# Kernel optimization log

Measured on AMD Instinct MI355X. Metric: run time of the kernel, lower is better.

Reference implementation:

```python
import jax, jax.numpy as jnp
import numpy as np

H = 32          # heads
E = 32          # head dim = mdl_channels // heads (must equal heads per module bug)
C = 1024        # mdl_channels == in_channels
MAXP = 128      # max_position_embeddings
EPS = 1e-5


def _layernorm(x, g, b):
    mu = jnp.mean(x, axis=-1, keepdims=True)
    var = jnp.var(x, axis=-1, keepdims=True)
    return (x - mu) * jax.lax.rsqrt(var + EPS) * g + b


def setup_inputs() -> dict:
    key = jax.random.key(0)
    ks = jax.random.split(key, 16)
    s = 0.02
    N, L = 4, 1024
    inp = {
        "x": jax.random.normal(ks[0], (N, L, C), jnp.float32),
        "Wq": jax.random.normal(ks[1], (C, C), jnp.float32) * s,
        "bq": jnp.zeros((C,), jnp.float32),
        "Wk": jax.random.normal(ks[2], (C, C), jnp.float32) * s,
        "bk": jnp.zeros((C,), jnp.float32),
        "Wv": jax.random.normal(ks[3], (C, C), jnp.float32) * s,
        "bv": jnp.zeros((C,), jnp.float32),
        "dist_emb": jax.random.normal(ks[4], (2 * MAXP + 1, E), jnp.float32) * s,
        "ln1_g": jnp.ones((C,), jnp.float32),
        "ln1_b": jnp.zeros((C,), jnp.float32),
        "ln2_g": jnp.ones((C,), jnp.float32),
        "ln2_b": jnp.zeros((C,), jnp.float32),
        "W1": jax.random.normal(ks[5], (C, C), jnp.float32) * s,
        "b1": jnp.zeros((C,), jnp.float32),
        "W2": jax.random.normal(ks[6], (C, C), jnp.float32) * s,
        "b2": jnp.zeros((C,), jnp.float32),
    }
    return inp


def reference(x, Wq, bq, Wk, bk, Wv, bv, dist_emb, ln1_g, ln1_b,
              ln2_g, ln2_b, W1, b1, W2, b2):
    N, L, _ = x.shape
    # QKV projections -> (N, L, H, E)
    q = (x @ Wq + bq).reshape(N, L, H, E)
    k = (x @ Wk + bk).reshape(N, L, H, E)
    v = (x @ Wv + bv).reshape(N, L, H, E)

    temp = 1.0 / np.sqrt(E).astype(np.float32)
    # content scores (N, H, L, S)
    QK = jnp.einsum('nlhe,nshe->nhls', q, k)
    # relative position scores (disentangled attention)
    pos = jnp.arange(L)
    dist = jnp.clip(pos[:, None] - pos[None, :], -MAXP, MAXP) + MAXP  # (L, L)
    pe = dist_emb[dist]                                              # (L, L, E)
    QK = QK + jnp.einsum('nlhe,lse->nhls', q, pe) \
            + jnp.einsum('nshe,lse->nhls', k, pe)
    A = jax.nn.softmax(temp * QK, axis=-1)          # dropout: eval mode (identity)
    t = jnp.einsum('nhls,nshe->nlhe', A, v).reshape(N, L, C)

    h = _layernorm(t + x, ln1_g, ln1_b)             # AddNorm (attention)
    m = jax.nn.relu(h @ W1 + b1) @ W2 + b2          # 2-layer MLP
    out = _layernorm(m + h, ln2_g, ln2_b)           # AddNorm (mlp)
    return jnp.swapaxes(out, 0, 1)                  # 'n f c -> f n c'
```

## Files before the change

### kernel.cpp

```cpp
#include <hip/hip_runtime.h>

#define H_ 32
#define E_ 32
#define C_ 1024
#define L_ 1024
#define N_ 4
#define M_ 4096
#define NH_ 128
#define D_ 257
#define DPAD 272
#define QDP 264
#define TEMP_ 0.17677669529663687f
#define QSCALE_ (TEMP_ * 1.4426950408889634f)

typedef unsigned short u16;
typedef __attribute__((ext_vector_type(8))) short short8;
typedef __attribute__((ext_vector_type(4))) float f32x4;
typedef __attribute__((ext_vector_type(4))) unsigned short u16x4;

__device__ __forceinline__ u16 f2bf(float f) {
  union { float f; unsigned u; } v; v.f = f;
  unsigned r = v.u + 0x7fffu + ((v.u >> 16) & 1u);
  return (u16)(r >> 16);
}
__device__ __forceinline__ float bf2f(u16 h) {
  union { unsigned u; float f; } v; v.u = ((unsigned)h) << 16;
  return v.f;
}
__device__ __forceinline__ f32x4 mfma16(short8 a, short8 b, f32x4 c) {
  return __builtin_amdgcn_mfma_f32_16x16x32_bf16(a, b, c, 0, 0, 0);
}
__device__ __forceinline__ float ex2(float x) {
#if __has_builtin(__builtin_amdgcn_exp2f)
  return __builtin_amdgcn_exp2f(x);
#else
  float r;
  asm("v_exp_f32 %0, %1\n\ts_nop 1" : "=v"(r) : "v"(x));
  return r;
#endif
}
__device__ __forceinline__ void gld16(const u16* g, u16* l) {
  __builtin_amdgcn_global_load_lds(
      (const __attribute__((address_space(1))) unsigned int*)g,
      (__attribute__((address_space(3))) unsigned int*)l, 16, 0, 0);
}

__global__ __launch_bounds__(256) void misc_kernel(
    const float* __restrict__ x, const float* __restrict__ demb,
    const float* __restrict__ bq, const float* __restrict__ bk,
    const float* __restrict__ bv, u16* __restrict__ xb,
    u16* __restrict__ demb_b, float* __restrict__ bqkv) {
  const int b = blockIdx.x, tid = threadIdx.x;
  if (b < 4096) {
    int i = b * 256 + tid;
    f32x4 v = reinterpret_cast<const f32x4*>(x)[i];
    u16x4 o2;
    o2[0] = f2bf(v[0]); o2[1] = f2bf(v[1]); o2[2] = f2bf(v[2]); o2[3] = f2bf(v[3]);
    reinterpret_cast<u16x4*>(xb)[i] = o2;
  } else {
    int i = (b - 4096) * 256 + tid;
    if (i < DPAD * E_) demb_b[i] = (i < D_ * E_) ? f2bf(demb[i]) : (u16)0;
    if (i < C_) { bqkv[i] = bq[i]; bqkv[C_ + i] = bk[i]; bqkv[2 * C_ + i] = bv[i]; }
  }
}

__global__ __launch_bounds__(256) void transpose_w_kernel(
    const float* __restrict__ Wq, const float* __restrict__ Wk,
    const float* __restrict__ Wv, const float* __restrict__ W1,
    const float* __restrict__ W2, u16* __restrict__ out_base) {
  __shared__ float tile[32][33];
  const int z = blockIdx.z;
  const float* in = (z == 0) ? Wq : (z == 1) ? Wk : (z == 2) ? Wv : (z == 3) ? W1 : W2;
  u16* out = out_base + (size_t)z * C_ * C_;
  int j0 = blockIdx.x * 32, c0 = blockIdx.y * 32;
#pragma unroll
  for (int i = 0; i < 4; ++i) {
    int cy = threadIdx.y + i * 8;
    tile[cy][threadIdx.x] = in[(size_t)(c0 + cy) * C_ + j0 + threadIdx.x];
  }
  __syncthreads();
#pragma unroll
  for (int i = 0; i < 4; ++i) {
    int jy = threadIdx.y + i * 8;
    out[(size_t)(j0 + jy) * C_ + c0 + threadIdx.x] = f2bf(tile[threadIdx.x][jy]);
  }
}

template <int EPI>
__global__ __launch_bounds__(256) void gemm128_kernel(
    const u16* __restrict__ A, const u16* __restrict__ Bt, int K,
    const float* __restrict__ bias,
    u16* __restrict__ out0, u16* __restrict__ out1, u16* __restrict__ out2) {
  __shared__ u16 As[128 * 64];
  __shared__ u16 Bs[128 * 64];
  const int bid = blockIdx.x;
  const int m0 = (bid & 31) << 7;
  const int n0 = (bid >> 5) << 7;
  const int tid = threadIdx.x;
  const int w = tid >> 6, lane = tid & 63, lhi = lane >> 4, llo = lane & 15;
  const int wr = w >> 1, wc = w & 1;
  const int w4 = w << 2;
  const int srow = lane >> 3, scol = (lane & 7) << 3;
  f32x4 acc[4][4] = {};
  for (int k0 = 0; k0 < K; k0 += 64) {
#pragma unroll
    for (int j = 0; j < 4; ++j) {
      const int seg = w4 + j;
      const int row = (seg << 3) + srow;
      gld16(&A[(size_t)(m0 + row) * K + k0 + scol], &As[seg << 9]);
      gld16(&Bt[(size_t)(n0 + row) * K + k0 + scol], &Bs[seg << 9]);
    }
    __syncthreads();
#pragma unroll
    for (int kk = 0; kk < 2; ++kk) {
      const int ko = (kk << 5) + lhi * 8;
      short8 af[4], bf[4];
#pragma unroll
      for (int mi = 0; mi < 4; ++mi)
        af[mi] = *reinterpret_cast<const short8*>(&As[(wr * 64 + mi * 16 + llo) * 64 + ko]);
#pragma unroll
      for (int ni = 0; ni < 4; ++ni)
        bf[ni] = *reinterpret_cast<const short8*>(&Bs[(wc * 64 + ni * 16 + llo) * 64 + ko]);
#pragma unroll
      for (int mi = 0; mi < 4; ++mi)
#pragma unroll
        for (int ni = 0; ni < 4; ++ni)
          acc[mi][ni] = mfma16(af[mi], bf[ni], acc[mi][ni]);
    }
    __syncthreads();
  }
#pragma unroll
  for (int mi = 0; mi < 4; ++mi)
#pragma unroll
    for (int ni = 0; ni < 4; ++ni)
#pragma unroll
      for (int r = 0; r < 4; ++r) {
        int row = m0 + wr * 64 + mi * 16 + lhi * 4 + r;
        int col = n0 + wc * 64 + ni * 16 + llo;
        float v = acc[mi][ni][r] + bias[col];
        if constexpr (EPI == 0) {
          int which = col >> 10, jj = col & 1023, h = jj >> 5, e2 = jj & 31;
          int n = row >> 10, l = row & 1023;
          int nh = (n << 5) | h;
          if (which == 0) v *= QSCALE_;
          u16 bvv = f2bf(v);
          if (which == 0)      out0[((size_t)((nh << 10) | l)) * 32 + e2] = bvv;
          else if (which == 1) out1[((size_t)((nh << 10) | l)) * 32 + e2] = bvv;
          else                 out2[(((size_t)(nh * 32 + e2)) << 10) | l] = bvv;
        } else if constexpr (EPI == 1) {
          out0[(size_t)row * C_ + col] = f2bf(fmaxf(v, 0.f));
        } else {
          out0[(size_t)row * C_ + col] = f2bf(v);
        }
      }
}

__global__ __launch_bounds__(256) void qdkd_kernel(
    const u16* __restrict__ src, const u16* __restrict__ demb,
    u16* __restrict__ dst, u16* __restrict__ aux0, u16* __restrict__ aux256) {
  const int wt = blockIdx.x * 4 + (threadIdx.x >> 6);
  const int lane = threadIdx.x & 63, lhi = lane >> 4, llo = lane & 15;
  const int m0 = wt << 4;
  short8 a = *reinterpret_cast<const short8*>(&src[(size_t)(m0 + llo) * E_ + lhi * 8]);
#pragma unroll
  for (int ct = 0; ct < 17; ++ct) {
    int d = ct * 16 + llo;
    short8 b = {0, 0, 0, 0, 0, 0, 0, 0};
    if (d < D_) b = *reinterpret_cast<const short8*>(&demb[d * E_ + lhi * 8]);
    f32x4 c = {};
    c = mfma16(a, b, c);
    if (d < D_) {
#pragma unroll
      for (int r = 0; r < 4; ++r) {
        u16 val = f2bf(c[r] * QSCALE_);
        dst[(size_t)(m0 + lhi * 4 + r) * D_ + d] = val;
        if (d == 0)   aux0[m0 + lhi * 4 + r] = val;
        if (d == 256) aux256[m0 + lhi * 4 + r] = val;
      }
    }
  }
}

__global__ __launch_bounds__(256) void attn_kernel(
    const u16* __restrict__ qw, const u16* __restrict__ kw,
    const u16* __restrict__ vT, const u16* __restrict__ dembp,
    const u16* __restrict__ KDg, const u16* __restrict__ kd0a,
    const u16* __restrict__ kd256a, u16* __restrict__ tb) {
  __shared__ u16 QDs[64 * QDP];
  __shared__ u16 kdc[2 * 1024];
  __shared__ u16 Pbuf[4 * 16 * 40];
  __shared__ float Lred[64];
  const int bid = blockIdx.x;
  const int nh = bid & (NH_ - 1);
  const int l0 = (bid >> 7) << 6;
  const int tid = threadIdx.x;
  const int w = tid >> 6, lane = tid & 63, lhi = lane >> 4, llo = lane & 15;
  const int lw0 = l0 + (w << 4);

  const u16* qb  = qw + (size_t)nh * (L_ * E_);
  const u16* kb  = kw + (size_t)nh * (L_ * E_);
  const u16* vb  = vT + (size_t)nh * (E_ * L_);
  const u16* kdg = KDg + (size_t)nh * ((size_t)L_ * D_);

  {
    const int side = tid >> 7, off = (tid & 127) * 8;
    const u16* srcA = (side ? kd256a : kd0a) + (size_t)nh * L_ + off;
    *reinterpret_cast<short8*>(&kdc[side * 1024 + off]) =
        *reinterpret_cast<const short8*>(srcA);
  }

  const short8 qA = *reinterpret_cast<const short8*>(&qb[(size_t)(lw0 + llo) * E_ + lhi * 8]);

#pragma unroll
  for (int dt = 0; dt < 17; ++dt) {
    short8 db = *reinterpret_cast<const short8*>(&dembp[(dt * 16 + llo) * E_ + lhi * 8]);
    f32x4 qd = {};
    qd = mfma16(qA, db, qd);
    const int qrow = (w << 4) + (lhi << 2);
#pragma unroll
    for (int r = 0; r < 4; ++r)
      QDs[(qrow + r) * QDP + dt * 16 + llo] = f2bf(qd[r]);
  }
  __syncthreads();

  const int qr4 = (w << 4) + (lhi << 2);
  float qdf0[4], qdf256[4];
#pragma unroll
  for (int r = 0; r < 4; ++r) {
    qdf0[r]   = bf2f(QDs[(qr4 + r) * QDP + 0]);
    qdf256[r] = bf2f(QDs[(qr4 + r) * QDP + 256]);
  }

  u16* Pw = &Pbuf[w * 16 * 40];
  f32x4 o0 = {}, o1 = {};
  float lacc[4] = {0.f, 0.f, 0.f, 0.f};

  for (int s0 = 0; s0 < L_; s0 += 32) {
    const int se = s0 + 2 * llo;
    short8 kB0 = *reinterpret_cast<const short8*>(&kb[(size_t)se * E_ + lhi * 8]);
    short8 kB1 = *reinterpret_cast<const short8*>(&kb[(size_t)(se + 1) * E_ + lhi * 8]);
    f32x4 st0 = {}, st1 = {};
    st0 = mfma16(qA, kB0, st0);
    st1 = mfma16(qA, kB1, st1);

    const int dmin = lw0 - s0 - 31, dmax = lw0 + 15 - s0;
    float p0[4], p1[4];
    if (dmin >= 128 || dmax <= -128) {
      const int sd = (dmin >= 128) ? 1 : 0;
      const float* qdf = sd ? qdf256 : qdf0;
      unsigned kc2 = *reinterpret_cast<const unsigned*>(&kdc[sd * 1024 + se]);
      const float kc0 = bf2f((u16)kc2), kc1 = bf2f((u16)(kc2 >> 16));
#pragma unroll
      for (int r = 0; r < 4; ++r) {
        p0[r] = ex2(st0[r] + qdf[r] + kc0);
        p1[r] = ex2(st1[r] + qdf[r] + kc1);
      }
    } else if (dmin >= -128 && dmax <= 128) {
      const int qoff = lw0 + (lhi << 2) + 128;
      u16x4 kd0v = *reinterpret_cast<const u16x4*>(&kdg[256 * se + qoff]);
      u16x4 kd1v = *reinterpret_cast<const u16x4*>(&kdg[256 * (se + 1) + qoff]);
#pragma unroll
      for (int r = 0; r < 4; ++r) {
        const int qq = lw0 + (lhi << 2) + r;
        float qd0 = bf2f(QDs[(qr4 + r) * QDP + (qq - se + 128)]);
        float qd1 = bf2f(QDs[(qr4 + r) * QDP + (qq - se + 127)]);
        p0[r] = ex2(st0[r] + qd0 + bf2f(kd0v[r]));
        p1[r] = ex2(st1[r] + qd1 + bf2f(kd1v[r]));
      }
    } else {
#pragma unroll
      for (int r = 0; r < 4; ++r) {
        const int qq = lw0 + (lhi << 2) + r;
        int d0 = qq - se;
        d0 = (d0 < -128 ? -128 : (d0 > 128 ? 128 : d0)) + 128;
        int d1 = qq - se - 1;
        d1 = (d1 < -128 ? -128 : (d1 > 128 ? 128 : d1)) + 128;
        float qd0 = bf2f(QDs[(qr4 + r) * QDP + d0]);
        float qd1 = bf2f(QDs[(qr4 + r) * QDP + d1]);
        float kd0 = bf2f(kdg[(size_t)se * D_ + d0]);
        float kd1 = bf2f(kdg[(size_t)(se + 1) * D_ + d1]);
        p0[r] = ex2(st0[r] + qd0 + kd0);
        p1[r] = ex2(st1[r] + qd1 + kd1);
      }
    }

#pragma unroll
    for (int r = 0; r < 4; ++r) {
      lacc[r] += p0[r] + p1[r];
      unsigned pw = (unsigned)f2bf(p0[r]) | ((unsigned)f2bf(p1[r]) << 16);
      *reinterpret_cast<unsigned*>(&Pw[((lhi << 2) + r) * 40 + 2 * llo]) = pw;
    }
    short8 pB = *reinterpret_cast<const short8*>(&Pw[llo * 40 + lhi * 8]);
    short8 vA0 = *reinterpret_cast<const short8*>(&vb[(size_t)llo * L_ + s0 + lhi * 8]);
    short8 vA1 = *reinterpret_cast<const short8*>(&vb[(size_t)(16 + llo) * L_ + s0 + lhi * 8]);
    o0 = mfma16(vA0, pB, o0);
    o1 = mfma16(vA1, pB, o1);
  }

#pragma unroll
  for (int r = 0; r < 4; ++r) {
    float t = lacc[r];
    t += __shfl_xor(t, 1); t += __shfl_xor(t, 2);
    t += __shfl_xor(t, 4); t += __shfl_xor(t, 8);
    if (llo == 0) Lred[(w << 4) + (lhi << 2) + r] = t;
  }
  const float inv = 1.0f / Lred[(w << 4) + llo];

  const int n = nh >> 5, h = nh & 31;
  const size_t obase = (((size_t)((n << 10) | (lw0 + llo))) * 32 + h) * 32;
  u16x4 w0, w1;
#pragma unroll
  for (int r = 0; r < 4; ++r) {
    w0[r] = f2bf(o0[r] * inv);
    w1[r] = f2bf(o1[r] * inv);
  }
  *reinterpret_cast<u16x4*>(&tb[obase + (lhi << 2)]) = w0;
  *reinterpret_cast<u16x4*>(&tb[obase + 16 + (lhi << 2)]) = w1;
}

__global__ __launch_bounds__(256) void ln1_kernel(
    const u16* __restrict__ tbuf, const float* __restrict__ x,
    const float* __restrict__ g, const float* __restrict__ b,
    u16* __restrict__ hb) {
  __shared__ float red[8];
  const int row = blockIdx.x, tid = threadIdx.x;
  const size_t base = (size_t)row * C_ + tid * 4;
  f32x4 xv = *reinterpret_cast<const f32x4*>(&x[base]);
  u16x4 tv = *reinterpret_cast<const u16x4*>(&tbuf[base]);
  float v[4]; float s1 = 0.f, s2 = 0.f;
#pragma unroll
  for (int i = 0; i < 4; ++i) {
    v[i] = xv[i] + bf2f(tv[i]);
    s1 += v[i]; s2 += v[i] * v[i];
  }
#pragma unroll
  for (int off = 32; off >= 1; off >>= 1) {
    s1 += __shfl_xor(s1, off); s2 += __shfl_xor(s2, off);
  }
  if ((tid & 63) == 0) { red[tid >> 6] = s1; red[4 + (tid >> 6)] = s2; }
  __syncthreads();
  float S1 = red[0] + red[1] + red[2] + red[3];
  float S2 = red[4] + red[5] + red[6] + red[7];
  float mu = S1 * (1.f / C_);
  float rs = rsqrtf(S2 * (1.f / C_) - mu * mu + 1e-5f);
#pragma unroll
  for (int i = 0; i < 4; ++i) {
    int c = tid * 4 + i;
    hb[base + i] = f2bf((v[i] - mu) * rs * g[c] + b[c]);
  }
}

__global__ __launch_bounds__(256) void ln2_kernel(
    const u16* __restrict__ mb, const u16* __restrict__ hb,
    const float* __restrict__ g, const float* __restrict__ b,
    float* __restrict__ out) {
  __shared__ float red[8];
  const int row = blockIdx.x, tid = threadIdx.x;
  const size_t base = (size_t)row * C_ + tid * 4;
  u16x4 mv = *reinterpret_cast<const u16x4*>(&mb[base]);
  u16x4 hv = *reinterpret_cast<const u16x4*>(&hb[base]);
  float v[4]; float s1 = 0.f, s2 = 0.f;
#pragma unroll
  for (int i = 0; i < 4; ++i) {
    v[i] = bf2f(mv[i]) + bf2f(hv[i]);
    s1 += v[i]; s2 += v[i] * v[i];
  }
#pragma unroll
  for (int off = 32; off >= 1; off >>= 1) {
    s1 += __shfl_xor(s1, off); s2 += __shfl_xor(s2, off);
  }
  if ((tid & 63) == 0) { red[tid >> 6] = s1; red[4 + (tid >> 6)] = s2; }
  __syncthreads();
  float S1 = red[0] + red[1] + red[2] + red[3];
  float S2 = red[4] + red[5] + red[6] + red[7];
  float mu = S1 * (1.f / C_);
  float rs = rsqrtf(S2 * (1.f / C_) - mu * mu + 1e-5f);
  const int n = row >> 10, l = row & 1023;
  const size_t ob = (size_t)(l * N_ + n) * C_ + tid * 4;
#pragma unroll
  for (int i = 0; i < 4; ++i) {
    int c = tid * 4 + i;
    out[ob + i] = (v[i] - mu) * rs * g[c] + b[c];
  }
}

extern "C" void kernel_launch(void* const* d_in, const int* in_sizes, int n_in,
                              void* d_out, int out_size, void* d_ws, size_t ws_size,
                              hipStream_t stream) {
  const float* x    = (const float*)d_in[0];
  const float* Wq   = (const float*)d_in[1];
  const float* bq   = (const float*)d_in[2];
  const float* Wk   = (const float*)d_in[3];
  const float* bk   = (const float*)d_in[4];
  const float* Wv   = (const float*)d_in[5];
  const float* bv   = (const float*)d_in[6];
  const float* demb = (const float*)d_in[7];
  const float* g1   = (const float*)d_in[8];
  const float* b1ln = (const float*)d_in[9];
  const float* g2   = (const float*)d_in[10];
  const float* b2ln = (const float*)d_in[11];
  const float* W1   = (const float*)d_in[12];
  const float* b1   = (const float*)d_in[13];
  const float* W2   = (const float*)d_in[14];
  const float* b2   = (const float*)d_in[15];
  float* outp = (float*)d_out;

  size_t o = 0;
  auto alloc = [&](size_t bytes) { size_t r = o; o += (bytes + 255) & ~(size_t)255; return r; };
  const size_t xb_o    = alloc((size_t)M_ * C_ * 2);
  const size_t wqkv_o  = alloc((size_t)3 * C_ * C_ * 2);
  const size_t w1_o    = alloc((size_t)C_ * C_ * 2);
  const size_t w2_o    = alloc((size_t)C_ * C_ * 2);
  const size_t bqkv_o  = alloc((size_t)3 * C_ * 4);
  const size_t demb_o  = alloc((size_t)DPAD * E_ * 2);
  const size_t q_o     = alloc((size_t)NH_ * L_ * E_ * 2);
  const size_t k_o     = alloc((size_t)NH_ * L_ * E_ * 2);
  const size_t vt_o    = alloc((size_t)NH_ * L_ * E_ * 2);
  const size_t kd_o    = alloc((size_t)NH_ * L_ * D_ * 2);
  const size_t kd0_o   = alloc((size_t)NH_ * L_ * 2);
  const size_t kd256_o = alloc((size_t)NH_ * L_ * 2);
  const size_t t_o     = alloc((size_t)M_ * C_ * 2);
  const size_t h_o     = alloc((size_t)M_ * C_ * 2);
  const size_t m1_o    = alloc((size_t)M_ * C_ * 2);
  const size_t m_o     = alloc((size_t)M_ * C_ * 2);
  if (o > ws_size) return;

  char* ws = (char*)d_ws;
  u16*   xb     = (u16*)(ws + xb_o);
  u16*   wqkv_t = (u16*)(ws + wqkv_o);
  u16*   w1_t   = (u16*)(ws + w1_o);
  u16*   w2_t   = (u16*)(ws + w2_o);
  float* bqkv   = (float*)(ws + bqkv_o);
  u16*   demb_b = (u16*)(ws + demb_o);
  u16*   q_ws   = (u16*)(ws + q_o);
  u16*   k_ws   = (u16*)(ws + k_o);
  u16*   vT_ws  = (u16*)(ws + vt_o);
  u16*   KD     = (u16*)(ws + kd_o);
  u16*   kd0a   = (u16*)(ws + kd0_o);
  u16*   kd256a = (u16*)(ws + kd256_o);
  u16*   t_b16  = (u16*)(ws + t_o);
  u16*   h_b16  = (u16*)(ws + h_o);
  u16*   m1_b16 = (u16*)(ws + m1_o);
  u16*   m_b16  = (u16*)(ws + m_o);

  misc_kernel<<<4096 + 34, 256, 0, stream>>>(x, demb, bq, bk, bv, xb, demb_b, bqkv);
  dim3 tb_(32, 8), tg_(32, 32, 5);
  transpose_w_kernel<<<tg_, tb_, 0, stream>>>(Wq, Wk, Wv, W1, W2, wqkv_t);

  gemm128_kernel<0><<<32 * 24, 256, 0, stream>>>(xb, wqkv_t, C_, bqkv, q_ws, k_ws, vT_ws);

  qdkd_kernel<<<2048, 256, 0, stream>>>(k_ws, demb_b, KD, kd0a, kd256a);

  attn_kernel<<<NH_ * 16, 256, 0, stream>>>(q_ws, k_ws, vT_ws, demb_b, KD, kd0a, kd256a, t_b16);

  ln1_kernel<<<M_, 256, 0, stream>>>(t_b16, x, g1, b1ln, h_b16);

  gemm128_kernel<1><<<32 * 8, 256, 0, stream>>>(h_b16, w1_t, C_, b1, m1_b16, nullptr, nullptr);
  gemm128_kernel<2><<<32 * 8, 256, 0, stream>>>(m1_b16, w2_t, C_, b2, m_b16, nullptr, nullptr);

  ln2_kernel<<<M_, 256, 0, stream>>>(m_b16, h_b16, g2, b2ln, outp);
}
```

Baseline: 311.8 us.

## Split attention key loop into region-specialized loops with register prefetch of K/V

Replaces the per-iteration branch over clipped/band/boundary distance regions with five consecutive loops whose bounds are computed up front, so each loop runs branch-free specialized code. K and V fragments for the next tile, plus the clipped-edge key-distance scalars, are prefetched into registers one iteration ahead to hide global load latency. The shared-memory kd cache and the __syncthreads are dropped, since each wave only reads its own QDs rows, and launch bounds request 4 blocks per CU. This costs more registers and code size, and the correctness of the region boundaries depends on careful index math.

```diff
diff --git a/kernel.cpp b/kernel.cpp
--- a/kernel.cpp
+++ b/kernel.cpp
@@ -181,13 +181,31 @@
   }
 }
 
-__global__ __launch_bounds__(256) void attn_kernel(
+
+#define PFKV(SN) { const int sc_ = (SN) > 992 ? 992 : (SN); const int se_ = sc_ + 2 * llo; \
+    kn0 = *(const short8*)&kb[(size_t)se_ * E_ + lhi * 8];                                 \
+    kn1 = *(const short8*)&kb[(size_t)(se_ + 1) * E_ + lhi * 8];                           \
+    vn0 = *(const short8*)&vb[(size_t)llo * L_ + sc_ + lhi * 8];                           \
+    vn1 = *(const short8*)&vb[(size_t)(16 + llo) * L_ + sc_ + lhi * 8]; }
+
+#define PVTAIL()                                                                           \
+    _Pragma("unroll") for (int r = 0; r < 4; ++r) {                                        \
+      lacc[r] += p0[r] + p1[r];                                                            \
+      unsigned pw_ = (unsigned)f2bf(p0[r]) | ((unsigned)f2bf(p1[r]) << 16);                \
+      *reinterpret_cast<unsigned*>(&Pw[((lhi << 2) + r) * 40 + 2 * llo]) = pw_;            \
+    }                                                                                      \
+    {                                                                                      \
+      short8 pB = *(const short8*)&Pw[llo * 40 + lhi * 8];                                 \
+      o0 = mfma16(vc0, pB, o0); o1 = mfma16(vc1, pB, o1);                                  \
+    }                                                                                      \
+    kc0 = kn0; kc1 = kn1; vc0 = vn0; vc1 = vn1;
+
+__global__ __launch_bounds__(256, 4) void attn_kernel(
     const u16* __restrict__ qw, const u16* __restrict__ kw,
     const u16* __restrict__ vT, const u16* __restrict__ dembp,
     const u16* __restrict__ KDg, const u16* __restrict__ kd0a,
     const u16* __restrict__ kd256a, u16* __restrict__ tb) {
   __shared__ u16 QDs[64 * QDP];
-  __shared__ u16 kdc[2 * 1024];
   __shared__ u16 Pbuf[4 * 16 * 40];
   __shared__ float Lred[64];
   const int bid = blockIdx.x;
@@ -201,29 +219,22 @@
   const u16* kb  = kw + (size_t)nh * (L_ * E_);
   const u16* vb  = vT + (size_t)nh * (E_ * L_);
   const u16* kdg = KDg + (size_t)nh * ((size_t)L_ * D_);
-
-  {
-    const int side = tid >> 7, off = (tid & 127) * 8;
-    const u16* srcA = (side ? kd256a : kd0a) + (size_t)nh * L_ + off;
-    *reinterpret_cast<short8*>(&kdc[side * 1024 + off]) =
-        *reinterpret_cast<const short8*>(srcA);
-  }
-
-  const short8 qA = *reinterpret_cast<const short8*>(&qb[(size_t)(lw0 + llo) * E_ + lhi * 8]);
+  const u16* k0g = kd0a + (size_t)nh * L_;
+  const u16* k2g = kd256a + (size_t)nh * L_;
+
+  const short8 qA = *(const short8*)&qb[(size_t)(lw0 + llo) * E_ + lhi * 8];
+  const int qr4 = (w << 4) + (lhi << 2);
 
 #pragma unroll
   for (int dt = 0; dt < 17; ++dt) {
-    short8 db = *reinterpret_cast<const short8*>(&dembp[(dt * 16 + llo) * E_ + lhi * 8]);
+    short8 db = *(const short8*)&dembp[(dt * 16 + llo) * E_ + lhi * 8];
     f32x4 qd = {};
     qd = mfma16(qA, db, qd);
-    const int qrow = (w << 4) + (lhi << 2);
 #pragma unroll
     for (int r = 0; r < 4; ++r)
-      QDs[(qrow + r) * QDP + dt * 16 + llo] = f2bf(qd[r]);
-  }
-  __syncthreads();
-
-  const int qr4 = (w << 4) + (lhi << 2);
+      QDs[(qr4 + r) * QDP + dt * 16 + llo] = f2bf(qd[r]);
+  }
+
   float qdf0[4], qdf256[4];
 #pragma unroll
   for (int r = 0; r < 4; ++r) {
@@ -231,70 +242,120 @@
     qdf256[r] = bf2f(QDs[(qr4 + r) * QDP + 256]);
   }
 
+  const int sMid0 = (lw0 >= 159) ? ((((lw0 - 159) >> 5) + 1) << 5) : 0;
+  const int sIB0  = (lw0 > 113) ? (((lw0 - 113 + 31) >> 5) << 5) : 0;
+  int sIB1 = (((lw0 + 97) >> 5) << 5) + 32; if (sIB1 > 1024) sIB1 = 1024;
+  int sFL  = ((lw0 + 143 + 31) >> 5) << 5;  if (sFL > 1024) sFL = 1024;
+
   u16* Pw = &Pbuf[w * 16 * 40];
   f32x4 o0 = {}, o1 = {};
   float lacc[4] = {0.f, 0.f, 0.f, 0.f};
 
-  for (int s0 = 0; s0 < L_; s0 += 32) {
+  short8 kc0, kc1, vc0, vc1, kn0, kn1, vn0, vn1;
+  {
+    const int se = 2 * llo;
+    kc0 = *(const short8*)&kb[(size_t)se * E_ + lhi * 8];
+    kc1 = *(const short8*)&kb[(size_t)(se + 1) * E_ + lhi * 8];
+    vc0 = *(const short8*)&vb[(size_t)llo * L_ + lhi * 8];
+    vc1 = *(const short8*)&vb[(size_t)(16 + llo) * L_ + lhi * 8];
+  }
+
+  int s0 = 0;
+  unsigned kcp = *(const unsigned*)&k2g[2 * llo];
+#pragma unroll 2
+  for (; s0 < sMid0; s0 += 32) {
+    PFKV(s0 + 32);
+    const int snc = (s0 + 32) > 992 ? 992 : (s0 + 32);
+    unsigned kcpn = *(const unsigned*)&k2g[snc + 2 * llo];
+    f32x4 st0 = {}, st1 = {};
+    st0 = mfma16(qA, kc0, st0); st1 = mfma16(qA, kc1, st1);
+    const float kf0 = bf2f((u16)kcp), kf1 = bf2f((u16)(kcp >> 16));
+    float p0[4], p1[4];
+#pragma unroll
+    for (int r = 0; r < 4; ++r) {
+      p0[r] = ex2(st0[r] + qdf256[r] + kf0);
+      p1[r] = ex2(st1[r] + qdf256[r] + kf1);
+    }
+    PVTAIL();
+    kcp = kcpn;
+  }
+  for (; s0 < sIB0; s0 += 32) {
+    PFKV(s0 + 32);
+    f32x4 st0 = {}, st1 = {};
+    st0 = mfma16(qA, kc0, st0); st1 = mfma16(qA, kc1, st1);
     const int se = s0 + 2 * llo;
-    short8 kB0 = *reinterpret_cast<const short8*>(&kb[(size_t)se * E_ + lhi * 8]);
-    short8 kB1 = *reinterpret_cast<const short8*>(&kb[(size_t)(se + 1) * E_ + lhi * 8]);
+    float p0[4], p1[4];
+#pragma unroll
+    for (int r = 0; r < 4; ++r) {
+      const int qq = lw0 + (lhi << 2) + r;
+      int d0 = qq - se;     d0 = (d0 < -128 ? -128 : (d0 > 128 ? 128 : d0)) + 128;
+      int d1 = qq - se - 1; d1 = (d1 < -128 ? -128 : (d1 > 128 ? 128 : d1)) + 128;
+      float qd0 = bf2f(QDs[(qr4 + r) * QDP + d0]);
+      float qd1 = bf2f(QDs[(qr4 + r) * QDP + d1]);
+      float kd0 = bf2f(kdg[(size_t)se * D_ + d0]);
+      float kd1 = bf2f(kdg[(size_t)(se + 1) * D_ + d1]);
+      p0[r] = ex2(st0[r] + qd0 + kd0);
+      p1[r] = ex2(st1[r] + qd1 + kd1);
+    }
+    PVTAIL();
+  }
+#pragma unroll 2
+  for (; s0 < sIB1; s0 += 32) {
+    PFKV(s0 + 32);
+    const int se = s0 + 2 * llo;
+    const int qoff = lw0 + (lhi << 2) + 128;
+    u16x4 kd0v = *(const u16x4*)&kdg[256 * se + qoff];
+    u16x4 kd1v = *(const u16x4*)&kdg[256 * se + 256 + qoff];
     f32x4 st0 = {}, st1 = {};
-    st0 = mfma16(qA, kB0, st0);
-    st1 = mfma16(qA, kB1, st1);
-
-    const int dmin = lw0 - s0 - 31, dmax = lw0 + 15 - s0;
+    st0 = mfma16(qA, kc0, st0); st1 = mfma16(qA, kc1, st1);
+    const int dbase = (lhi << 2) + (lw0 - s0) - 2 * llo + 128;
     float p0[4], p1[4];
-    if (dmin >= 128 || dmax <= -128) {
-      const int sd = (dmin >= 128) ? 1 : 0;
-      const float* qdf = sd ? qdf256 : qdf0;
-      unsigned kc2 = *reinterpret_cast<const unsigned*>(&kdc[sd * 1024 + se]);
-      const float kc0 = bf2f((u16)kc2), kc1 = bf2f((u16)(kc2 >> 16));
-#pragma unroll
-      for (int r = 0; r < 4; ++r) {
-        p0[r] = ex2(st0[r] + qdf[r] + kc0);
-        p1[r] = ex2(st1[r] + qdf[r] + kc1);
-      }
-    } else if (dmin >= -128 && dmax <= 128) {
-      const int qoff = lw0 + (lhi << 2) + 128;
-      u16x4 kd0v = *reinterpret_cast<const u16x4*>(&kdg[256 * se + qoff]);
-      u16x4 kd1v = *reinterpret_cast<const u16x4*>(&kdg[256 * (se + 1) + qoff]);
-#pragma unroll
-      for (int r = 0; r < 4; ++r) {
-        const int qq = lw0 + (lhi << 2) + r;
-        float qd0 = bf2f(QDs[(qr4 + r) * QDP + (qq - se + 128)]);
-        float qd1 = bf2f(QDs[(qr4 + r) * QDP + (qq - se + 127)]);
-        p0[r] = ex2(st0[r] + qd0 + bf2f(kd0v[r]));
-        p1[r] = ex2(st1[r] + qd1 + bf2f(kd1v[r]));
-      }
-    } else {
-#pragma unroll
-      for (int r = 0; r < 4; ++r) {
-        const int qq = lw0 + (lhi << 2) + r;
-        int d0 = qq - se;
-        d0 = (d0 < -128 ? -128 : (d0 > 128 ? 128 : d0)) + 128;
-        int d1 = qq - se - 1;
-        d1 = (d1 < -128 ? -128 : (d1 > 128 ? 128 : d1)) + 128;
-        float qd0 = bf2f(QDs[(qr4 + r) * QDP + d0]);
-        float qd1 = bf2f(QDs[(qr4 + r) * QDP + d1]);
-        float kd0 = bf2f(kdg[(size_t)se * D_ + d0]);
-        float kd1 = bf2f(kdg[(size_t)(se + 1) * D_ + d1]);
-        p0[r] = ex2(st0[r] + qd0 + kd0);
-        p1[r] = ex2(st1[r] + qd1 + kd1);
-      }
-    }
-
 #pragma unroll
     for (int r = 0; r < 4; ++r) {
-      lacc[r] += p0[r] + p1[r];
-      unsigned pw = (unsigned)f2bf(p0[r]) | ((unsigned)f2bf(p1[r]) << 16);
-      *reinterpret_cast<unsigned*>(&Pw[((lhi << 2) + r) * 40 + 2 * llo]) = pw;
-    }
-    short8 pB = *reinterpret_cast<const short8*>(&Pw[llo * 40 + lhi * 8]);
-    short8 vA0 = *reinterpret_cast<const short8*>(&vb[(size_t)llo * L_ + s0 + lhi * 8]);
-    short8 vA1 = *reinterpret_cast<const short8*>(&vb[(size_t)(16 + llo) * L_ + s0 + lhi * 8]);
-    o0 = mfma16(vA0, pB, o0);
-    o1 = mfma16(vA1, pB, o1);
+      float qd0 = bf2f(QDs[(qr4 + r) * QDP + dbase + r]);
+      float qd1 = bf2f(QDs[(qr4 + r) * QDP + dbase + r - 1]);
+      p0[r] = ex2(st0[r] + qd0 + bf2f(kd0v[r]));
+      p1[r] = ex2(st1[r] + qd1 + bf2f(kd1v[r]));
+    }
+    PVTAIL();
+  }
+  for (; s0 < sFL; s0 += 32) {
+    PFKV(s0 + 32);
+    f32x4 st0 = {}, st1 = {};
+    st0 = mfma16(qA, kc0, st0); st1 = mfma16(qA, kc1, st1);
+    const int se = s0 + 2 * llo;
+    float p0[4], p1[4];
+#pragma unroll
+    for (int r = 0; r < 4; ++r) {
+      const int qq = lw0 + (lhi << 2) + r;
+      int d0 = qq - se;     d0 = (d0 < -128 ? -128 : (d0 > 128 ? 128 : d0)) + 128;
+      int d1 = qq - se - 1; d1 = (d1 < -128 ? -128 : (d1 > 128 ? 128 : d1)) + 128;
+      float qd0 = bf2f(QDs[(qr4 + r) * QDP + d0]);
+      float qd1 = bf2f(QDs[(qr4 + r) * QDP + d1]);
+      float kd0 = bf2f(kdg[(size_t)se * D_ + d0]);
+      float kd1 = bf2f(kdg[(size_t)(se + 1) * D_ + d1]);
+      p0[r] = ex2(st0[r] + qd0 + kd0);
+      p1[r] = ex2(st1[r] + qd1 + kd1);
+    }
+    PVTAIL();
+  }
+  kcp = *(const unsigned*)&k0g[(s0 > 992 ? 992 : s0) + 2 * llo];
+#pragma unroll 2
+  for (; s0 < 1024; s0 += 32) {
+    PFKV(s0 + 32);
+    const int snc = (s0 + 32) > 992 ? 992 : (s0 + 32);
+    unsigned kcpn = *(const unsigned*)&k0g[snc + 2 * llo];
+    f32x4 st0 = {}, st1 = {};
+    st0 = mfma16(qA, kc0, st0); st1 = mfma16(qA, kc1, st1);
+    const float kf0 = bf2f((u16)kcp), kf1 = bf2f((u16)(kcp >> 16));
+    float p0[4], p1[4];
+#pragma unroll
+    for (int r = 0; r < 4; ++r) {
+      p0[r] = ex2(st0[r] + qdf0[r] + kf0);
+      p1[r] = ex2(st1[r] + qdf0[r] + kf1);
+    }
+    PVTAIL();
+    kcp = kcpn;
   }
 
 #pragma unroll
```

Result: faster. 300.8 us (-3.5%).

## Double-buffer K/V tiles in LDS and software-pipeline the attention PV MFMA

Applied to the files above, without the earlier changes.

The attention kernel now stages K and V tiles into shared memory with a double-buffered async load (gld16), prefetching the next tile while computing the current one. The PV MFMA is deferred by one iteration so it overlaps with the next score computation. Region boundaries for the relative-position branches are precomputed per wave, bf16 packing uses a cheaper rounding, and launch bounds request 3 blocks per CU. The cost is an extra __syncthreads per iteration and more LDS use. Boundary tiles are now classified by wave rather than by block, and the rounding mode of P changes slightly.

```diff
diff --git a/kernel.cpp b/kernel.cpp
--- a/kernel.cpp
+++ b/kernel.cpp
@@ -181,13 +181,14 @@
   }
 }
 
-__global__ __launch_bounds__(256) void attn_kernel(
+__global__ __launch_bounds__(256, 3) void attn_kernel(
     const u16* __restrict__ qw, const u16* __restrict__ kw,
     const u16* __restrict__ vT, const u16* __restrict__ dembp,
     const u16* __restrict__ KDg, const u16* __restrict__ kd0a,
     const u16* __restrict__ kd256a, u16* __restrict__ tb) {
   __shared__ u16 QDs[64 * QDP];
-  __shared__ u16 kdc[2 * 1024];
+  __shared__ u16 Ksh[2][1024];
+  __shared__ u16 Vsh[2][1024];
   __shared__ u16 Pbuf[4 * 16 * 40];
   __shared__ float Lred[64];
   const int bid = blockIdx.x;
@@ -201,29 +202,32 @@
   const u16* kb  = kw + (size_t)nh * (L_ * E_);
   const u16* vb  = vT + (size_t)nh * (E_ * L_);
   const u16* kdg = KDg + (size_t)nh * ((size_t)L_ * D_);
-
-  {
-    const int side = tid >> 7, off = (tid & 127) * 8;
-    const u16* srcA = (side ? kd256a : kd0a) + (size_t)nh * L_ + off;
-    *reinterpret_cast<short8*>(&kdc[side * 1024 + off]) =
-        *reinterpret_cast<const short8*>(srcA);
-  }
-
-  const short8 qA = *reinterpret_cast<const short8*>(&qb[(size_t)(lw0 + llo) * E_ + lhi * 8]);
+  const u16* k0g = kd0a + (size_t)nh * L_;
+  const u16* k2g = kd256a + (size_t)nh * L_;
+
+  const u16* stgb;
+  if (w < 2) stgb = kb + (size_t)(2 * (lane & 15) + (w & 1)) * E_ + (lane >> 4) * 8;
+  else       stgb = vb + (size_t)((w & 1) * 16 + (lane & 15)) * L_ + (lane >> 4) * 8;
+  u16* stgd[2];
+  stgd[0] = (w < 2 ? &Ksh[0][0] : &Vsh[0][0]) + (w & 1) * 512;
+  stgd[1] = (w < 2 ? &Ksh[1][0] : &Vsh[1][0]) + (w & 1) * 512;
+  const int kstride = (w < 2) ? E_ : 1;
+
+  gld16(stgb, stgd[0]);
+
+  const short8 qA = *(const short8*)&qb[(size_t)(lw0 + llo) * E_ + lhi * 8];
+  const int qr4 = (w << 4) + (lhi << 2);
 
 #pragma unroll
   for (int dt = 0; dt < 17; ++dt) {
-    short8 db = *reinterpret_cast<const short8*>(&dembp[(dt * 16 + llo) * E_ + lhi * 8]);
+    short8 db = *(const short8*)&dembp[(dt * 16 + llo) * E_ + lhi * 8];
     f32x4 qd = {};
     qd = mfma16(qA, db, qd);
-    const int qrow = (w << 4) + (lhi << 2);
 #pragma unroll
     for (int r = 0; r < 4; ++r)
-      QDs[(qrow + r) * QDP + dt * 16 + llo] = f2bf(qd[r]);
-  }
-  __syncthreads();
-
-  const int qr4 = (w << 4) + (lhi << 2);
+      QDs[(qr4 + r) * QDP + dt * 16 + llo] = f2bf(qd[r]);
+  }
+
   float qdf0[4], qdf256[4];
 #pragma unroll
   for (int r = 0; r < 4; ++r) {
@@ -231,70 +235,111 @@
     qdf256[r] = bf2f(QDs[(qr4 + r) * QDP + 256]);
   }
 
+  const int sMid0 = (lw0 >= 159) ? ((((lw0 - 159) >> 5) + 1) << 5) : 0;
+  const int sIB0  = (lw0 > 113) ? (((lw0 - 113 + 31) >> 5) << 5) : 0;
+  int sIB1 = (((lw0 + 97) >> 5) << 5) + 32; if (sIB1 > 1024) sIB1 = 1024;
+  int sFL  = ((lw0 + 143 + 31) >> 5) << 5;  if (sFL > 1024) sFL = 1024;
+
   u16* Pw = &Pbuf[w * 16 * 40];
   f32x4 o0 = {}, o1 = {};
   float lacc[4] = {0.f, 0.f, 0.f, 0.f};
-
-  for (int s0 = 0; s0 < L_; s0 += 32) {
-    const int se = s0 + 2 * llo;
-    short8 kB0 = *reinterpret_cast<const short8*>(&kb[(size_t)se * E_ + lhi * 8]);
-    short8 kB1 = *reinterpret_cast<const short8*>(&kb[(size_t)(se + 1) * E_ + lhi * 8]);
+  short8 vp0, vp1;
+
+  __syncthreads();
+
+#define ASSEMBLE(T, ST0, ST1, P0, P1)                                          \
+  {                                                                            \
+    const int t_ = (T);                                                        \
+    if (t_ < sMid0) {                                                          \
+      unsigned kc2 = *(const unsigned*)&k2g[t_ + 2 * llo];                     \
+      const float kf0 = bf2f((u16)kc2), kf1 = bf2f((u16)(kc2 >> 16));          \
+      _Pragma("unroll") for (int r = 0; r < 4; ++r) {                          \
+        P0[r] = ex2(ST0[r] + qdf256[r] + kf0);                                 \
+        P1[r] = ex2(ST1[r] + qdf256[r] + kf1);                                 \
+      }                                                                        \
+    } else if (t_ < sIB0 || (t_ >= sIB1 && t_ < sFL)) {                        \
+      const int se = t_ + 2 * llo;                                             \
+      _Pragma("unroll") for (int r = 0; r < 4; ++r) {                          \
+        const int qq = lw0 + (lhi << 2) + r;                                   \
+        int d0 = qq - se;     d0 = (d0 < -128 ? -128 : (d0 > 128 ? 128 : d0)) + 128; \
+        int d1 = qq - se - 1; d1 = (d1 < -128 ? -128 : (d1 > 128 ? 128 : d1)) + 128; \
+        float qd0 = bf2f(QDs[(qr4 + r) * QDP + d0]);                           \
+        float qd1 = bf2f(QDs[(qr4 + r) * QDP + d1]);                           \
+        float kd0 = bf2f(kdg[(size_t)se * D_ + d0]);                           \
+        float kd1 = bf2f(kdg[(size_t)(se + 1) * D_ + d1]);                     \
+        P0[r] = ex2(ST0[r] + qd0 + kd0);                                       \
+        P1[r] = ex2(ST1[r] + qd1 + kd1);                                       \
+      }                                                                        \
+    } else if (t_ < sIB1) {                                                    \
+      const int se = t_ + 2 * llo;                                             \
+      const int qoff = lw0 + (lhi << 2) + 128;                                 \
+      u16x4 kd0v = *(const u16x4*)&kdg[256 * se + qoff];                       \
+      u16x4 kd1v = *(const u16x4*)&kdg[256 * se + 256 + qoff];                 \
+      const int dbase = (lhi << 2) + (lw0 - t_) - 2 * llo + 128;               \
+      _Pragma("unroll") for (int r = 0; r < 4; ++r) {                          \
+        float qd0 = bf2f(QDs[(qr4 + r) * QDP + dbase + r]);                    \
+        float qd1 = bf2f(QDs[(qr4 + r) * QDP + dbase + r - 1]);                \
+        P0[r] = ex2(ST0[r] + qd0 + bf2f(kd0v[r]));                             \
+        P1[r] = ex2(ST1[r] + qd1 + bf2f(kd1v[r]));                             \
+      }                                                                        \
+    } else {                                                                   \
+      unsigned kc2 = *(const unsigned*)&k0g[t_ + 2 * llo];                     \
+      const float kf0 = bf2f((u16)kc2), kf1 = bf2f((u16)(kc2 >> 16));          \
+      _Pragma("unroll") for (int r = 0; r < 4; ++r) {                          \
+        P0[r] = ex2(ST0[r] + qdf0[r] + kf0);                                   \
+        P1[r] = ex2(ST1[r] + qdf0[r] + kf1);                                   \
+      }                                                                        \
+    }                                                                          \
+  }
+
+#define PACKW(P0, P1)                                                          \
+  _Pragma("unroll") for (int r = 0; r < 4; ++r) {                              \
+    lacc[r] += P0[r] + P1[r];                                                  \
+    union { float f; unsigned u; } a0_, a1_; a0_.f = P0[r]; a1_.f = P1[r];     \
+    unsigned pw_ = ((a0_.u + 0x8000u) >> 16) | ((a1_.u + 0x8000u) & 0xffff0000u); \
+    *reinterpret_cast<unsigned*>(&Pw[((lhi << 2) + r) * 40 + 2 * llo]) = pw_;  \
+  }
+
+  {
+    gld16(stgb + 32 * kstride, stgd[1]);
+    short8 kc0 = *(const short8*)&Ksh[0][lane * 8];
+    short8 kc1 = *(const short8*)&Ksh[0][512 + lane * 8];
+    vp0 = *(const short8*)&Vsh[0][lane * 8];
+    vp1 = *(const short8*)&Vsh[0][512 + lane * 8];
     f32x4 st0 = {}, st1 = {};
-    st0 = mfma16(qA, kB0, st0);
-    st1 = mfma16(qA, kB1, st1);
-
-    const int dmin = lw0 - s0 - 31, dmax = lw0 + 15 - s0;
+    st0 = mfma16(qA, kc0, st0); st1 = mfma16(qA, kc1, st1);
     float p0[4], p1[4];
-    if (dmin >= 128 || dmax <= -128) {
-      const int sd = (dmin >= 128) ? 1 : 0;
-      const float* qdf = sd ? qdf256 : qdf0;
-      unsigned kc2 = *reinterpret_cast<const unsigned*>(&kdc[sd * 1024 + se]);
-      const float kc0 = bf2f((u16)kc2), kc1 = bf2f((u16)(kc2 >> 16));
-#pragma unroll
-      for (int r = 0; r < 4; ++r) {
-        p0[r] = ex2(st0[r] + qdf[r] + kc0);
-        p1[r] = ex2(st1[r] + qdf[r] + kc1);
-      }
-    } else if (dmin >= -128 && dmax <= 128) {
-      const int qoff = lw0 + (lhi << 2) + 128;
-      u16x4 kd0v = *reinterpret_cast<const u16x4*>(&kdg[256 * se + qoff]);
-      u16x4 kd1v = *reinterpret_cast<const u16x4*>(&kdg[256 * (se + 1) + qoff]);
-#pragma unroll
-      for (int r = 0; r < 4; ++r) {
-        const int qq = lw0 + (lhi << 2) + r;
-        float qd0 = bf2f(QDs[(qr4 + r) * QDP + (qq - se + 128)]);
-        float qd1 = bf2f(QDs[(qr4 + r) * QDP + (qq - se + 127)]);
-        p0[r] = ex2(st0[r] + qd0 + bf2f(kd0v[r]));
-        p1[r] = ex2(st1[r] + qd1 + bf2f(kd1v[r]));
-      }
-    } else {
-#pragma unroll
-      for (int r = 0; r < 4; ++r) {
-        const int qq = lw0 + (lhi << 2) + r;
-        int d0 = qq - se;
-        d0 = (d0 < -128 ? -128 : (d0 > 128 ? 128 : d0)) + 128;
-        int d1 = qq - se - 1;
-        d1 = (d1 < -128 ? -128 : (d1 > 128 ? 128 : d1)) + 128;
-        float qd0 = bf2f(QDs[(qr4 + r) * QDP + d0]);
-        float qd1 = bf2f(QDs[(qr4 + r) * QDP + d1]);
-        float kd0 = bf2f(kdg[(size_t)se * D_ + d0]);
-        float kd1 = bf2f(kdg[(size_t)(se + 1) * D_ + d1]);
-        p0[r] = ex2(st0[r] + qd0 + kd0);
-        p1[r] = ex2(st1[r] + qd1 + kd1);
-      }
+    ASSEMBLE(0, st0, st1, p0, p1);
+    PACKW(p0, p1);
+    __syncthreads();
+  }
+
+  for (int t = 32; t < 1024; t += 32) {
+    const int buf = (t >> 5) & 1;
+    const int snext = (t + 32 > 992) ? 992 : (t + 32);
+    gld16(stgb + snext * kstride, stgd[buf ^ 1]);
+    short8 kc0 = *(const short8*)&Ksh[buf][lane * 8];
+    short8 kc1 = *(const short8*)&Ksh[buf][512 + lane * 8];
+    short8 vc0 = *(const short8*)&Vsh[buf][lane * 8];
+    short8 vc1 = *(const short8*)&Vsh[buf][512 + lane * 8];
+    f32x4 st0 = {}, st1 = {};
+    st0 = mfma16(qA, kc0, st0); st1 = mfma16(qA, kc1, st1);
+    {
+      short8 pB = *(const short8*)&Pw[llo * 40 + lhi * 8];
+      o0 = mfma16(vp0, pB, o0);
+      o1 = mfma16(vp1, pB, o1);
     }
-
-#pragma unroll
-    for (int r = 0; r < 4; ++r) {
-      lacc[r] += p0[r] + p1[r];
-      unsigned pw = (unsigned)f2bf(p0[r]) | ((unsigned)f2bf(p1[r]) << 16);
-      *reinterpret_cast<unsigned*>(&Pw[((lhi << 2) + r) * 40 + 2 * llo]) = pw;
-    }
-    short8 pB = *reinterpret_cast<const short8*>(&Pw[llo * 40 + lhi * 8]);
-    short8 vA0 = *reinterpret_cast<const short8*>(&vb[(size_t)llo * L_ + s0 + lhi * 8]);
-    short8 vA1 = *reinterpret_cast<const short8*>(&vb[(size_t)(16 + llo) * L_ + s0 + lhi * 8]);
-    o0 = mfma16(vA0, pB, o0);
-    o1 = mfma16(vA1, pB, o1);
+    float p0[4], p1[4];
+    ASSEMBLE(t, st0, st1, p0, p1);
+    PACKW(p0, p1);
+    vp0 = vc0; vp1 = vc1;
+    __syncthreads();
+  }
+
+  {
+    short8 pB = *(const short8*)&Pw[llo * 40 + lhi * 8];
+    o0 = mfma16(vp0, pB, o0);
+    o1 = mfma16(vp1, pB, o1);
   }
 
 #pragma unroll
@@ -316,6 +361,8 @@
   }
   *reinterpret_cast<u16x4*>(&tb[obase + (lhi << 2)]) = w0;
   *reinterpret_cast<u16x4*>(&tb[obase + 16 + (lhi << 2)]) = w1;
+#undef ASSEMBLE
+#undef PACKW
 }
 
 __global__ __launch_bounds__(256) void ln1_kernel(
```

Result: slower. 404.6 us (+29.8%).

## Transpose attention score MFMA so each lane owns a query row

Applied to the files above, without the earlier changes.

The score MFMA now takes K as the A operand and Q as the B operand. Each lane therefore holds a single query row, and the softmax row sum reduces with two cross-lane shuffles instead of an LDS reduction. The LDS staging of the clamped key-distance columns and the block barrier are removed, the P tile uses an XOR-swizzled LDS layout with a cheaper bf16 rounding, and launch bounds request higher occupancy. In exchange, the dedicated unclamped middle-band path is dropped, so those tiles go through the generic clamped path with scattered global loads.

```diff
diff --git a/kernel.cpp b/kernel.cpp
--- a/kernel.cpp
+++ b/kernel.cpp
@@ -181,141 +181,126 @@
   }
 }
 
-__global__ __launch_bounds__(256) void attn_kernel(
+__global__ __launch_bounds__(256, 4) void attn_kernel(
     const u16* __restrict__ qw, const u16* __restrict__ kw,
     const u16* __restrict__ vT, const u16* __restrict__ dembp,
     const u16* __restrict__ KDg, const u16* __restrict__ kd0a,
     const u16* __restrict__ kd256a, u16* __restrict__ tb) {
   __shared__ u16 QDs[64 * QDP];
-  __shared__ u16 kdc[2 * 1024];
-  __shared__ u16 Pbuf[4 * 16 * 40];
-  __shared__ float Lred[64];
+  __shared__ u16 Pbuf[4 * 512];
   const int bid = blockIdx.x;
   const int nh = bid & (NH_ - 1);
   const int l0 = (bid >> 7) << 6;
   const int tid = threadIdx.x;
   const int w = tid >> 6, lane = tid & 63, lhi = lane >> 4, llo = lane & 15;
   const int lw0 = l0 + (w << 4);
+  const int lg = lw0 + llo;
+  const int lrow = (w << 4) + llo;
 
   const u16* qb  = qw + (size_t)nh * (L_ * E_);
   const u16* kb  = kw + (size_t)nh * (L_ * E_);
   const u16* vb  = vT + (size_t)nh * (E_ * L_);
   const u16* kdg = KDg + (size_t)nh * ((size_t)L_ * D_);
-
-  {
-    const int side = tid >> 7, off = (tid & 127) * 8;
-    const u16* srcA = (side ? kd256a : kd0a) + (size_t)nh * L_ + off;
-    *reinterpret_cast<short8*>(&kdc[side * 1024 + off]) =
-        *reinterpret_cast<const short8*>(srcA);
-  }
-
-  const short8 qA = *reinterpret_cast<const short8*>(&qb[(size_t)(lw0 + llo) * E_ + lhi * 8]);
-
-#pragma unroll
-  for (int dt = 0; dt < 17; ++dt) {
-    short8 db = *reinterpret_cast<const short8*>(&dembp[(dt * 16 + llo) * E_ + lhi * 8]);
+  const u16* k0g = kd0a + (size_t)nh * L_;
+  const u16* k2g = kd256a + (size_t)nh * L_;
+
+  const short8 qA = *(const short8*)&qb[(size_t)lg * E_ + lhi * 8];
+  const int qr4 = (w << 4) + (lhi << 2);
+
+#pragma unroll
+  for (int dt = 0; dt < 16; ++dt) {
+    short8 db = *(const short8*)&dembp[(dt * 16 + llo) * E_ + lhi * 8];
     f32x4 qd = {};
     qd = mfma16(qA, db, qd);
-    const int qrow = (w << 4) + (lhi << 2);
 #pragma unroll
     for (int r = 0; r < 4; ++r)
-      QDs[(qrow + r) * QDP + dt * 16 + llo] = f2bf(qd[r]);
-  }
-  __syncthreads();
-
-  const int qr4 = (w << 4) + (lhi << 2);
-  float qdf0[4], qdf256[4];
-#pragma unroll
-  for (int r = 0; r < 4; ++r) {
-    qdf0[r]   = bf2f(QDs[(qr4 + r) * QDP + 0]);
-    qdf256[r] = bf2f(QDs[(qr4 + r) * QDP + 256]);
-  }
-
-  u16* Pw = &Pbuf[w * 16 * 40];
+      QDs[(qr4 + r) * QDP + dt * 16 + llo] = f2bf(qd[r]);
+  }
+  {
+    short8 db = *(const short8*)&dembp[(size_t)(256 + llo) * E_ + lhi * 8];
+    f32x4 qd = {};
+    qd = mfma16(qA, db, qd);
+    if (llo == 0) {
+#pragma unroll
+      for (int r = 0; r < 4; ++r)
+        QDs[(qr4 + r) * QDP + 256] = f2bf(qd[r]);
+    }
+  }
+
+  const float qd0   = bf2f(QDs[lrow * QDP + 0]);
+  const float qd256 = bf2f(QDs[lrow * QDP + 256]);
+
   f32x4 o0 = {}, o1 = {};
-  float lacc[4] = {0.f, 0.f, 0.f, 0.f};
+  float lacc = 0.f;
+  char* Pw = reinterpret_cast<char*>(&Pbuf[w * 512]);
 
   for (int s0 = 0; s0 < L_; s0 += 32) {
-    const int se = s0 + 2 * llo;
-    short8 kB0 = *reinterpret_cast<const short8*>(&kb[(size_t)se * E_ + lhi * 8]);
-    short8 kB1 = *reinterpret_cast<const short8*>(&kb[(size_t)(se + 1) * E_ + lhi * 8]);
+    short8 kA0 = *(const short8*)&kb[(size_t)(s0 + llo) * E_ + lhi * 8];
+    short8 kA1 = *(const short8*)&kb[(size_t)(s0 + 16 + llo) * E_ + lhi * 8];
     f32x4 st0 = {}, st1 = {};
-    st0 = mfma16(qA, kB0, st0);
-    st1 = mfma16(qA, kB1, st1);
-
-    const int dmin = lw0 - s0 - 31, dmax = lw0 + 15 - s0;
-    float p0[4], p1[4];
-    if (dmin >= 128 || dmax <= -128) {
-      const int sd = (dmin >= 128) ? 1 : 0;
-      const float* qdf = sd ? qdf256 : qdf0;
-      unsigned kc2 = *reinterpret_cast<const unsigned*>(&kdc[sd * 1024 + se]);
-      const float kc0 = bf2f((u16)kc2), kc1 = bf2f((u16)(kc2 >> 16));
+    st0 = mfma16(kA0, qA, st0);
+    st1 = mfma16(kA1, qA, st1);
+
+    float p[8];
+    const bool far_hi = (lw0 - (s0 + 31)) >= 128;
+    const bool far_lo = (s0 - (lw0 + 15)) >= 128;
+    if (far_hi || far_lo) {
+      const float qdc = far_hi ? qd256 : qd0;
+      const u16* kcg = far_hi ? k2g : k0g;
+      u16x4 kc0 = *(const u16x4*)&kcg[s0 + lhi * 4];
+      u16x4 kc1 = *(const u16x4*)&kcg[s0 + 16 + lhi * 4];
 #pragma unroll
       for (int r = 0; r < 4; ++r) {
-        p0[r] = ex2(st0[r] + qdf[r] + kc0);
-        p1[r] = ex2(st1[r] + qdf[r] + kc1);
-      }
-    } else if (dmin >= -128 && dmax <= 128) {
-      const int qoff = lw0 + (lhi << 2) + 128;
-      u16x4 kd0v = *reinterpret_cast<const u16x4*>(&kdg[256 * se + qoff]);
-      u16x4 kd1v = *reinterpret_cast<const u16x4*>(&kdg[256 * (se + 1) + qoff]);
-#pragma unroll
-      for (int r = 0; r < 4; ++r) {
-        const int qq = lw0 + (lhi << 2) + r;
-        float qd0 = bf2f(QDs[(qr4 + r) * QDP + (qq - se + 128)]);
-        float qd1 = bf2f(QDs[(qr4 + r) * QDP + (qq - se + 127)]);
-        p0[r] = ex2(st0[r] + qd0 + bf2f(kd0v[r]));
-        p1[r] = ex2(st1[r] + qd1 + bf2f(kd1v[r]));
+        p[r]     = ex2(st0[r] + qdc + bf2f(kc0[r]));
+        p[4 + r] = ex2(st1[r] + qdc + bf2f(kc1[r]));
       }
     } else {
 #pragma unroll
-      for (int r = 0; r < 4; ++r) {
-        const int qq = lw0 + (lhi << 2) + r;
-        int d0 = qq - se;
-        d0 = (d0 < -128 ? -128 : (d0 > 128 ? 128 : d0)) + 128;
-        int d1 = qq - se - 1;
-        d1 = (d1 < -128 ? -128 : (d1 > 128 ? 128 : d1)) + 128;
-        float qd0 = bf2f(QDs[(qr4 + r) * QDP + d0]);
-        float qd1 = bf2f(QDs[(qr4 + r) * QDP + d1]);
-        float kd0 = bf2f(kdg[(size_t)se * D_ + d0]);
-        float kd1 = bf2f(kdg[(size_t)(se + 1) * D_ + d1]);
-        p0[r] = ex2(st0[r] + qd0 + kd0);
-        p1[r] = ex2(st1[r] + qd1 + kd1);
+      for (int i = 0; i < 2; ++i)
+#pragma unroll
+        for (int r = 0; r < 4; ++r) {
+          const int scol = s0 + i * 16 + lhi * 4 + r;
+          int d = lg - scol;
+          d = (d < -128 ? -128 : (d > 128 ? 128 : d)) + 128;
+          float qd = bf2f(QDs[lrow * QDP + d]);
+          float kd = bf2f(kdg[(size_t)scol * D_ + d]);
+          p[i * 4 + r] = ex2((i ? st1[r] : st0[r]) + qd + kd);
+        }
+    }
+    lacc += ((p[0] + p[1]) + (p[2] + p[3])) + ((p[4] + p[5]) + (p[6] + p[7]));
+
+#pragma unroll
+    for (int i = 0; i < 2; ++i)
+#pragma unroll
+      for (int b = 0; b < 2; ++b) {
+        union { float f; unsigned u; } a0, a1;
+        a0.f = p[i * 4 + 2 * b]; a1.f = p[i * 4 + 2 * b + 1];
+        unsigned wv = ((a0.u + 0x8000u) >> 16) | ((a1.u + 0x8000u) & 0xffff0000u);
+        int u = (i * 4 + lhi) ^ (llo & 6);
+        *reinterpret_cast<unsigned*>(Pw + llo * 64 + u * 8 + b * 4) = wv;
       }
-    }
-
-#pragma unroll
-    for (int r = 0; r < 4; ++r) {
-      lacc[r] += p0[r] + p1[r];
-      unsigned pw = (unsigned)f2bf(p0[r]) | ((unsigned)f2bf(p1[r]) << 16);
-      *reinterpret_cast<unsigned*>(&Pw[((lhi << 2) + r) * 40 + 2 * llo]) = pw;
-    }
-    short8 pB = *reinterpret_cast<const short8*>(&Pw[llo * 40 + lhi * 8]);
-    short8 vA0 = *reinterpret_cast<const short8*>(&vb[(size_t)llo * L_ + s0 + lhi * 8]);
-    short8 vA1 = *reinterpret_cast<const short8*>(&vb[(size_t)(16 + llo) * L_ + s0 + lhi * 8]);
+    short8 pB = *reinterpret_cast<const short8*>(
+        Pw + llo * 64 + (((lhi * 2) ^ (llo & 6)) * 8));
+    short8 vA0 = *(const short8*)&vb[(size_t)llo * L_ + s0 + lhi * 8];
+    short8 vA1 = *(const short8*)&vb[(size_t)(16 + llo) * L_ + s0 + lhi * 8];
     o0 = mfma16(vA0, pB, o0);
     o1 = mfma16(vA1, pB, o1);
   }
 
-#pragma unroll
-  for (int r = 0; r < 4; ++r) {
-    float t = lacc[r];
-    t += __shfl_xor(t, 1); t += __shfl_xor(t, 2);
-    t += __shfl_xor(t, 4); t += __shfl_xor(t, 8);
-    if (llo == 0) Lred[(w << 4) + (lhi << 2) + r] = t;
-  }
-  const float inv = 1.0f / Lred[(w << 4) + llo];
+  float l2 = lacc + __shfl_xor(lacc, 16);
+  float lt = l2 + __shfl_xor(l2, 32);
+  const float inv = 1.0f / lt;
 
   const int n = nh >> 5, h = nh & 31;
-  const size_t obase = (((size_t)((n << 10) | (lw0 + llo))) * 32 + h) * 32;
+  const size_t obase = (((size_t)((n << 10) | lg)) * 32 + h) * 32;
   u16x4 w0, w1;
 #pragma unroll
   for (int r = 0; r < 4; ++r) {
     w0[r] = f2bf(o0[r] * inv);
     w1[r] = f2bf(o1[r] * inv);
   }
-  *reinterpret_cast<u16x4*>(&tb[obase + (lhi << 2)]) = w0;
-  *reinterpret_cast<u16x4*>(&tb[obase + 16 + (lhi << 2)]) = w1;
+  *reinterpret_cast<u16x4*>(&tb[obase + lhi * 4]) = w0;
+  *reinterpret_cast<u16x4*>(&tb[obase + 16 + lhi * 4]) = w1;
 }
 
 __global__ __launch_bounds__(256) void ln1_kernel(
```

New measurement: 270.0 us. 1.15x faster.
